# Performance work log

Hardware: AMD Instinct MI355X
Metric: run time of the kernel (lower is better)

Reference implementation:

```python
import jax, jax.numpy as jnp
import numpy as np

FS = 16000.0
Q = 2.0
MAX_MFC = 150.0
LP_CUTOFF = 2.5
ATT_FACTOR = 1.0  # dau1997 preset


def _mfc_array():
    # mfc = 0 (lowpass), 5, 10 Hz linear, then log-spaced with ratio r up to max_mfc
    mfc = [0.0, 5.0, 10.0]
    r = (1.0 + 1.0 / (2.0 * Q)) / (1.0 - 1.0 / (2.0 * Q))  # = 5/3 for Q=2
    f = 10.0 * r
    while f <= MAX_MFC:
        mfc.append(f)
        f *= r
    return np.array(mfc, dtype=np.float64)  # 8 entries for the defaults


def _butter2_lp(fcut, fs):
    # 2nd-order Butterworth lowpass via bilinear transform (matches scipy.signal.butter)
    K = np.tan(np.pi * fcut / fs)
    n = 1.0 / (1.0 + np.sqrt(2.0) * K + K * K)
    b = np.array([K * K, 2.0 * K * K, K * K]) * n
    a = np.array([1.0, 2.0 * (K * K - 1.0) * n, (1.0 - np.sqrt(2.0) * K + K * K) * n])
    return b, a


def setup_inputs() -> dict:
    key = jax.random.key(0)
    x = jax.random.normal(key, (4, 31, 48000), dtype=jnp.float32)  # [B, F, T]
    return {"x": x}


def reference(x):
    B, F, T = x.shape
    N = B * F
    xr = x.reshape(N, T)

    # ---- mfc = 0 filter: 2nd-order Butterworth lowpass @ 2.5 Hz, DF2T scan ----
    b_np, a_np = _butter2_lp(LP_CUTOFF, FS)
    b = jnp.asarray(b_np, jnp.float32)
    a = jnp.asarray(a_np, jnp.float32)

    def lp_step(state, xt):  # state [N,2], xt [N]
        y = b[0] * xt + state[:, 0]
        s0 = b[1] * xt - a[1] * y + state[:, 1]
        s1 = b[2] * xt - a[2] * y
        return jnp.stack([s0, s1], axis=1), y

    _, ylp = jax.lax.scan(lp_step, jnp.zeros((N, 2), jnp.float32), xr.T)
    ylp = 2.0 * ylp.T  # [N, T], factor 2 = 6 dB emphasis

    # ---- bandpass efilt: complex first-order resonators ----
    mfc = _mfc_array()[1:]                      # [M] bandpass center freqs
    bw = np.where(mfc <= 10.0, 5.0, mfc / Q)    # 5 Hz bandwidth for linear part
    e0 = np.exp(-np.pi * bw / FS)               # exp(-(2*pi*bw/fs)/2)
    b0 = jnp.asarray((1.0 - e0).astype(np.complex64))
    cpole = jnp.asarray((e0 * np.exp(1j * 2.0 * np.pi * mfc / FS)).astype(np.complex64))
    M = mfc.shape[0]

    def bp_step(yprev, xt):  # yprev [N,M] complex, xt [N] complex
        y = b0[None, :] * xt[:, None] + cpole[None, :] * yprev
        return y, y

    _, ybp = jax.lax.scan(bp_step, jnp.zeros((N, M), jnp.complex64),
                          xr.T.astype(jnp.complex64))
    ybp = 2.0 * jnp.moveaxis(ybp, 0, -1)        # [N, M, T]

    # phase preserved for mfc <= 10 Hz (real part), envelope (abs) above
    keep_phase = jnp.asarray(mfc <= 10.0)
    out_bp = jnp.where(keep_phase[None, :, None], jnp.real(ybp), ATT_FACTOR * jnp.abs(ybp))

    out = jnp.concatenate([ylp[:, None, :], out_bp], axis=1)  # [N, 1+M, T]
    return out.reshape(B, F, 1 + M, T)
```

## Files before the change

kernel.cpp:

```cpp
#include <hip/hip_runtime.h>
#include <cmath>

#define T_LEN 48000
#define L_CHUNK 128
#define N_CHUNKS 375
#define N_ROWS 124
#define SLOTS 1024
#define ROWS_PER_BLK 64
#define XS_STRIDE 132
#define TR_STRIDE 20
#define GRP 15
#define NGRP 25

struct CoefF {
    float lp_b0, lp_b1, lp_b2, lp_a1, lp_a2;
    float bp_b0[7], bp_cr[7], bp_ci[7];
};
struct CoefD {
    double p00, p01, p10, p11;
    double Pr[7], Pi[7];
};

__device__ __forceinline__ void sel_M(int ch, const CoefD& D,
                                      double& m00, double& m01, double& m10, double& m11) {
    if (ch == 0) {
        m00 = D.p00; m01 = D.p01; m10 = D.p10; m11 = D.p11;
    } else {
        double Pr = 0.0, Pi = 0.0;
#pragma unroll
        for (int c = 1; c < 8; ++c) if (ch == c) { Pr = D.Pr[c - 1]; Pi = D.Pi[c - 1]; }
        m00 = Pr; m01 = -Pi; m10 = Pi; m11 = Pr;
    }
}

template <bool FINAL>
__global__ __launch_bounds__(512) void mfb_chunk(const float* __restrict__ x,
                                                 CoefF C, CoefD D,
                                                 float2* __restrict__ ws_fin,
                                                 const float2* __restrict__ U,
                                                 float* __restrict__ out) {
    extern __shared__ __align__(16) float smem[];
    float* xs = smem;
    const int t     = threadIdx.x;
    const int j     = blockIdx.y;
    const int n0    = (int)blockIdx.x * ROWS_PER_BLK;
    const int tbase = j * L_CHUNK;

#pragma unroll
    for (int i = 0; i < 4; ++i) {
        int g = i * 512 + t;
        int r = g >> 5, c = (g & 31) * 4;
        int n = n0 + r;
        float4 v = make_float4(0.f, 0.f, 0.f, 0.f);
        if (n < N_ROWS)
            v = *reinterpret_cast<const float4*>(x + (size_t)n * T_LEN + tbase + c);
        *reinterpret_cast<float4*>(xs + r * XS_STRIDE + c) = v;
    }
    __syncthreads();

    const int ch   = t >> 6;
    const int nn   = t & 63;
    const int n    = n0 + nn;
    const int slot = ch * 128 + n;
    float* trw = smem + ROWS_PER_BLK * XS_STRIDE + ch * (64 * TR_STRIDE);

    float f_b0, f_b1 = 0.f, f_b2 = 0.f, f_a1 = 0.f, f_a2 = 0.f, f_cr = 0.f, f_ci = 0.f;
    if (ch == 0) {
        f_b0 = C.lp_b0; f_b1 = C.lp_b1; f_b2 = C.lp_b2; f_a1 = C.lp_a1; f_a2 = C.lp_a2;
    } else {
        f_b0 = 0.f;
#pragma unroll
        for (int c = 1; c < 8; ++c)
            if (ch == c) { f_b0 = C.bp_b0[c - 1]; f_cr = C.bp_cr[c - 1]; f_ci = C.bp_ci[c - 1]; }
    }
    const bool kp = (ch <= 2);

    float s0 = 0.f, s1 = 0.f;
    if (FINAL) {
        const int g = j / GRP, i = j - g * GRP;
        double m00, m01, m10, m11;
        sel_M(ch, D, m00, m01, m10, m11);
        float2 ug = U[(size_t)g * SLOTS + slot];
        double u0 = ug.x, u1 = ug.y;
        const float2* Fb = ws_fin + (size_t)(g * GRP) * SLOTS + slot;
        float2 f[GRP - 1];
#pragma unroll
        for (int k = 0; k < GRP - 1; ++k)
            f[k] = (k < i) ? Fb[(size_t)k * SLOTS] : make_float2(0.f, 0.f);
#pragma unroll
        for (int k = 0; k < GRP - 1; ++k)
            if (k < i) {
                double t0 = (double)f[k].x + m00 * u0 + m01 * u1;
                double t1 = (double)f[k].y + m10 * u0 + m11 * u1;
                u0 = t0; u1 = t1;
            }
        s0 = (float)u0; s1 = (float)u1;
    }

    for (int b = 0; b < L_CHUNK / 16; ++b) {
        float4 xv4[4];
#pragma unroll
        for (int q = 0; q < 4; ++q)
            xv4[q] = *reinterpret_cast<const float4*>(xs + nn * XS_STRIDE + b * 16 + q * 4);
        const float* xv = reinterpret_cast<const float*>(xv4);

        float buf[16];
        if (ch == 0) {
#pragma unroll
            for (int k = 0; k < 16; ++k) {
                float xvk = xv[k];
                float y  = fmaf(f_b0, xvk, s0);
                s0 = fmaf(f_b1, xvk, fmaf(-f_a1, y, s1));
                s1 = fmaf(f_b2, xvk, -f_a2 * y);
                if (FINAL) buf[k] = 2.0f * y;
            }
        } else {
#pragma unroll
            for (int k = 0; k < 16; ++k) {
                float xvk = xv[k];
                float nyr = fmaf(f_cr, s0, fmaf(-f_ci, s1, f_b0 * xvk));
                float nyi = fmaf(f_cr, s1, f_ci * s0);
                s0 = nyr; s1 = nyi;
                if (FINAL)
                    buf[k] = kp ? 2.0f * nyr : 2.0f * sqrtf(fmaf(nyr, nyr, nyi * nyi));
            }
        }

        if (FINAL) {
            asm volatile("" ::: "memory");
            *reinterpret_cast<float4*>(trw + nn * TR_STRIDE + 0)  = make_float4(buf[0], buf[1], buf[2], buf[3]);
            *reinterpret_cast<float4*>(trw + nn * TR_STRIDE + 4)  = make_float4(buf[4], buf[5], buf[6], buf[7]);
            *reinterpret_cast<float4*>(trw + nn * TR_STRIDE + 8)  = make_float4(buf[8], buf[9], buf[10], buf[11]);
            *reinterpret_cast<float4*>(trw + nn * TR_STRIDE + 12) = make_float4(buf[12], buf[13], buf[14], buf[15]);
            asm volatile("" ::: "memory");
#pragma unroll
            for (int s = 0; s < 4; ++s) {
                int rr = s * 16 + (nn >> 2);
                int kk = (nn & 3) * 4;
                int nrow = n0 + rr;
                if (nrow < N_ROWS) {
                    float4 v = *reinterpret_cast<const float4*>(trw + rr * TR_STRIDE + kk);
                    *reinterpret_cast<float4*>(out + (size_t)(nrow * 8 + ch) * T_LEN
                                               + tbase + b * 16 + kk) = v;
                }
            }
        }
    }
    if (!FINAL) ws_fin[(size_t)j * SLOTS + slot] = make_float2(s0, s1);
}

__global__ __launch_bounds__(256) void mfb_groupsum(const float2* __restrict__ ws_fin,
                                                    float2* __restrict__ A, CoefD D) {
    int tid = blockIdx.x * 256 + (int)threadIdx.x;
    int s = tid & 1023, g = tid >> 10;
    double m00, m01, m10, m11;
    sel_M(s >> 7, D, m00, m01, m10, m11);

    const float2* base = ws_fin + (size_t)g * GRP * SLOTS + s;
    float2 f[GRP];
#pragma unroll
    for (int i = 0; i < GRP; ++i) f[i] = base[(size_t)i * SLOTS];

    double a0 = 0.0, a1 = 0.0;
#pragma unroll
    for (int i = 0; i < GRP; ++i) {
        double t0 = m00 * a0 + m01 * a1 + (double)f[i].x;
        double t1 = m10 * a0 + m11 * a1 + (double)f[i].y;
        a0 = t0; a1 = t1;
    }
    A[(size_t)g * SLOTS + s] = make_float2((float)a0, (float)a1);
}

__global__ __launch_bounds__(256) void mfb_groupscan(const float2* __restrict__ A,
                                                     float2* __restrict__ U, CoefD D15) {
    int s = blockIdx.x * 256 + (int)threadIdx.x;
    double m00, m01, m10, m11;
    sel_M(s >> 7, D15, m00, m01, m10, m11);

    float2 f[NGRP];
#pragma unroll
    for (int g = 0; g < NGRP; ++g) f[g] = A[(size_t)g * SLOTS + s];

    double u0 = 0.0, u1 = 0.0;
#pragma unroll
    for (int g = 0; g < NGRP; ++g) {
        U[(size_t)g * SLOTS + s] = make_float2((float)u0, (float)u1);
        double t0 = (double)f[g].x + m00 * u0 + m01 * u1;
        double t1 = (double)f[g].y + m10 * u0 + m11 * u1;
        u0 = t0; u1 = t1;
    }
}

extern "C" void kernel_launch(void* const* d_in, const int* in_sizes, int n_in,
                              void* d_out, int out_size, void* d_ws, size_t ws_size,
                              hipStream_t stream) {
    const float* x = (const float*)d_in[0];
    float* out = (float*)d_out;
    char* ws = (char*)d_ws;
    float2* ws_fin  = (float2*)ws;
    float2* Agg     = (float2*)(ws + 3072000);
    float2* Upre    = (float2*)(ws + 3276800);

    const double PI = 3.141592653589793;
    const double FS = 16000.0;
    CoefF C; CoefD D, D15;
    {
        double K   = tan(PI * 2.5 / FS);
        double nrm = 1.0 / (1.0 + sqrt(2.0) * K + K * K);
        double a1  = 2.0 * (K * K - 1.0) * nrm;
        double a2  = (1.0 - sqrt(2.0) * K + K * K) * nrm;
        C.lp_b0 = (float)(K * K * nrm);
        C.lp_b1 = (float)(2.0 * K * K * nrm);
        C.lp_b2 = (float)(K * K * nrm);
        C.lp_a1 = (float)a1;
        C.lp_a2 = (float)a2;
        double p00 = -a1, p01 = 1.0, p10 = -a2, p11 = 0.0;
        for (int i = 0; i < 7; ++i) {
            double q00 = p00 * p00 + p01 * p10, q01 = p00 * p01 + p01 * p11;
            double q10 = p10 * p00 + p11 * p10, q11 = p10 * p01 + p11 * p11;
            p00 = q00; p01 = q01; p10 = q10; p11 = q11;
        }
        D.p00 = p00; D.p01 = p01; D.p10 = p10; D.p11 = p11;
        double r00 = 1, r01 = 0, r10 = 0, r11 = 1, b00 = p00, b01 = p01, b10 = p10, b11 = p11;
        for (int e = 15; e > 0; e >>= 1) {
            if (e & 1) {
                double q00 = r00 * b00 + r01 * b10, q01 = r00 * b01 + r01 * b11;
                double q10 = r10 * b00 + r11 * b10, q11 = r10 * b01 + r11 * b11;
                r00 = q00; r01 = q01; r10 = q10; r11 = q11;
            }
            double q00 = b00 * b00 + b01 * b10, q01 = b00 * b01 + b01 * b11;
            double q10 = b10 * b00 + b11 * b10, q11 = b10 * b01 + b11 * b11;
            b00 = q00; b01 = q01; b10 = q10; b11 = q11;
        }
        D15.p00 = r00; D15.p01 = r01; D15.p10 = r10; D15.p11 = r11;

        double rr = (1.0 + 1.0 / 4.0) / (1.0 - 1.0 / 4.0);
        double mfc[7]; mfc[0] = 5.0; mfc[1] = 10.0;
        double f = 10.0 * rr;
        for (int m = 2; m < 7; ++m) { mfc[m] = f; f *= rr; }
        for (int m = 0; m < 7; ++m) {
            double bw = (mfc[m] <= 10.0) ? 5.0 : mfc[m] * 0.5;
            double e0 = exp(-PI * bw / FS);
            double th = 2.0 * PI * mfc[m] / FS;
            C.bp_b0[m] = (float)(1.0 - e0);
            C.bp_cr[m] = (float)(e0 * cos(th));
            C.bp_ci[m] = (float)(e0 * sin(th));
            double eL  = exp(-PI * bw * (double)L_CHUNK / FS);
            double ang = th * (double)L_CHUNK;
            D.Pr[m] = eL * cos(ang);
            D.Pi[m] = eL * sin(ang);
            double eG  = exp(-PI * bw * (double)(L_CHUNK * GRP) / FS);
            double angG = th * (double)(L_CHUNK * GRP);
            D15.Pr[m] = eG * cos(angG);
            D15.Pi[m] = eG * sin(angG);
        }
    }

    const int smem1 = ROWS_PER_BLK * XS_STRIDE * 4;
    const int smem3 = smem1 + 8 * 64 * TR_STRIDE * 4;
    dim3 grid(2, N_CHUNKS);
    mfb_chunk<false><<<grid, 512, smem1, stream>>>(x, C, D, ws_fin, nullptr, nullptr);
    mfb_groupsum<<<100, 256, 0, stream>>>(ws_fin, Agg, D);
    mfb_groupscan<<<4, 256, 0, stream>>>(Agg, Upre, D15);
    mfb_chunk<true><<<grid, 512, smem3, stream>>>(x, C, D, ws_fin, Upre, out);
}
```

Baseline: 69.96 us.

## Restructure output pass so each wave writes long contiguous runs per stream

The final pass is split into its own kernel. Each 64-lane wave now handles one (row, channel) stream over a window of 64 consecutive chunks, with one lane per chunk. It reads x directly from global with register double-buffering, stages results in LDS, and then writes 32 KB contiguous float4 runs per output row. The old scheme wrote only 64-byte fragments per row per step. The change targets output write coalescing and removes the shared x tile and the template branching. In exchange, x loads become strided per lane, and tail lanes in the last window sit idle.

```diff
diff --git a/kernel.cpp b/kernel.cpp
--- a/kernel.cpp
+++ b/kernel.cpp
@@ -8,9 +8,12 @@
 #define SLOTS 1024
 #define ROWS_PER_BLK 64
 #define XS_STRIDE 132
-#define TR_STRIDE 20
+#define TILE_STRIDE 132
 #define GRP 15
 #define NGRP 25
+#define N_STREAM 992
+#define N_WIN 6
+#define WIN 64
 
 struct CoefF {
     float lp_b0, lp_b1, lp_b2, lp_a1, lp_a2;
@@ -33,12 +36,23 @@
     }
 }
 
-template <bool FINAL>
-__global__ __launch_bounds__(512) void mfb_chunk(const float* __restrict__ x,
-                                                 CoefF C, CoefD D,
-                                                 float2* __restrict__ ws_fin,
-                                                 const float2* __restrict__ U,
-                                                 float* __restrict__ out) {
+__device__ __forceinline__ void sel_coef(int ch, const CoefF& C,
+                                         float& b0, float& b1, float& b2, float& a1,
+                                         float& a2, float& cr, float& ci) {
+    b1 = b2 = a1 = a2 = cr = ci = 0.f;
+    if (ch == 0) {
+        b0 = C.lp_b0; b1 = C.lp_b1; b2 = C.lp_b2; a1 = C.lp_a1; a2 = C.lp_a2;
+    } else {
+        b0 = 0.f;
+#pragma unroll
+        for (int c = 1; c < 8; ++c)
+            if (ch == c) { b0 = C.bp_b0[c - 1]; cr = C.bp_cr[c - 1]; ci = C.bp_ci[c - 1]; }
+    }
+}
+
+__global__ __launch_bounds__(512) void mfb_p1(const float* __restrict__ x,
+                                              CoefF C,
+                                              float2* __restrict__ ws_fin) {
     extern __shared__ __align__(16) float smem[];
     float* xs = smem;
     const int t     = threadIdx.x;
@@ -58,25 +72,101 @@
     }
     __syncthreads();
 
-    const int ch   = t >> 6;
-    const int nn   = t & 63;
-    const int n    = n0 + nn;
+    const int ch = t >> 6, nn = t & 63;
+    const int n  = n0 + nn;
+
+    float f_b0, f_b1, f_b2, f_a1, f_a2, f_cr, f_ci;
+    sel_coef(ch, C, f_b0, f_b1, f_b2, f_a1, f_a2, f_cr, f_ci);
+
+    float s0 = 0.f, s1 = 0.f;
+    for (int b = 0; b < L_CHUNK / 16; ++b) {
+        float4 xv4[4];
+#pragma unroll
+        for (int q = 0; q < 4; ++q)
+            xv4[q] = *reinterpret_cast<const float4*>(xs + nn * XS_STRIDE + b * 16 + q * 4);
+        const float* xv = reinterpret_cast<const float*>(xv4);
+        if (ch == 0) {
+#pragma unroll
+            for (int k = 0; k < 16; ++k) {
+                float xvk = xv[k];
+                float y  = fmaf(f_b0, xvk, s0);
+                s0 = fmaf(f_b1, xvk, fmaf(-f_a1, y, s1));
+                s1 = fmaf(f_b2, xvk, -f_a2 * y);
+            }
+        } else {
+#pragma unroll
+            for (int k = 0; k < 16; ++k) {
+                float xvk = xv[k];
+                float nyr = fmaf(f_cr, s0, fmaf(-f_ci, s1, f_b0 * xvk));
+                float nyi = fmaf(f_cr, s1, f_ci * s0);
+                s0 = nyr; s1 = nyi;
+            }
+        }
+    }
+    ws_fin[(size_t)j * SLOTS + ch * 128 + n] = make_float2(s0, s1);
+}
+
+__global__ __launch_bounds__(256) void mfb_groupsum(const float2* __restrict__ ws_fin,
+                                                    float2* __restrict__ A, CoefD D) {
+    int tid = blockIdx.x * 256 + (int)threadIdx.x;
+    int s = tid & 1023, g = tid >> 10;
+    double m00, m01, m10, m11;
+    sel_M(s >> 7, D, m00, m01, m10, m11);
+    const float2* base = ws_fin + (size_t)g * GRP * SLOTS + s;
+    float2 f[GRP];
+#pragma unroll
+    for (int i = 0; i < GRP; ++i) f[i] = base[(size_t)i * SLOTS];
+    double a0 = 0.0, a1 = 0.0;
+#pragma unroll
+    for (int i = 0; i < GRP; ++i) {
+        double t0 = m00 * a0 + m01 * a1 + (double)f[i].x;
+        double t1 = m10 * a0 + m11 * a1 + (double)f[i].y;
+        a0 = t0; a1 = t1;
+    }
+    A[(size_t)g * SLOTS + s] = make_float2((float)a0, (float)a1);
+}
+
+__global__ __launch_bounds__(256) void mfb_groupscan(const float2* __restrict__ A,
+                                                     float2* __restrict__ U, CoefD D15) {
+    int s = blockIdx.x * 256 + (int)threadIdx.x;
+    double m00, m01, m10, m11;
+    sel_M(s >> 7, D15, m00, m01, m10, m11);
+    float2 f[NGRP];
+#pragma unroll
+    for (int g = 0; g < NGRP; ++g) f[g] = A[(size_t)g * SLOTS + s];
+    double u0 = 0.0, u1 = 0.0;
+#pragma unroll
+    for (int g = 0; g < NGRP; ++g) {
+        U[(size_t)g * SLOTS + s] = make_float2((float)u0, (float)u1);
+        double t0 = (double)f[g].x + m00 * u0 + m01 * u1;
+        double t1 = (double)f[g].y + m10 * u0 + m11 * u1;
+        u0 = t0; u1 = t1;
+    }
+}
+
+__global__ __launch_bounds__(128) void mfb_out(const float* __restrict__ x,
+                                               CoefF C, CoefD D,
+                                               const float2* __restrict__ ws_fin,
+                                               const float2* __restrict__ U,
+                                               float* __restrict__ out) {
+    extern __shared__ __align__(16) float smem[];
+    const int wv = (int)threadIdx.x >> 6, L = (int)threadIdx.x & 63;
+    const int unit = (int)blockIdx.x * 2 + wv;
+    float* tile = smem + wv * (WIN * TILE_STRIDE);
+
+    const int sid = unit / N_WIN;
+    const int w   = unit - sid * N_WIN;
+    const int n   = sid >> 3, ch = sid & 7;
     const int slot = ch * 128 + n;
-    float* trw = smem + ROWS_PER_BLK * XS_STRIDE + ch * (64 * TR_STRIDE);
-
-    float f_b0, f_b1 = 0.f, f_b2 = 0.f, f_a1 = 0.f, f_a2 = 0.f, f_cr = 0.f, f_ci = 0.f;
-    if (ch == 0) {
-        f_b0 = C.lp_b0; f_b1 = C.lp_b1; f_b2 = C.lp_b2; f_a1 = C.lp_a1; f_a2 = C.lp_a2;
-    } else {
-        f_b0 = 0.f;
-#pragma unroll
-        for (int c = 1; c < 8; ++c)
-            if (ch == c) { f_b0 = C.bp_b0[c - 1]; f_cr = C.bp_cr[c - 1]; f_ci = C.bp_ci[c - 1]; }
-    }
+    const int j   = w * WIN + L;
+    const bool act = j < N_CHUNKS;
+
+    float f_b0, f_b1, f_b2, f_a1, f_a2, f_cr, f_ci;
+    sel_coef(ch, C, f_b0, f_b1, f_b2, f_a1, f_a2, f_cr, f_ci);
     const bool kp = (ch <= 2);
 
     float s0 = 0.f, s1 = 0.f;
-    if (FINAL) {
+    if (act) {
         const int g = j / GRP, i = j - g * GRP;
         double m00, m01, m10, m11;
         sel_M(ch, D, m00, m01, m10, m11);
@@ -97,13 +187,21 @@
         s0 = (float)u0; s1 = (float)u1;
     }
 
-    for (int b = 0; b < L_CHUNK / 16; ++b) {
-        float4 xv4[4];
+    const float* xrow = x + (size_t)n * T_LEN + (size_t)j * L_CHUNK;
+    float4 cur[4] = {};
+    if (act) {
 #pragma unroll
         for (int q = 0; q < 4; ++q)
-            xv4[q] = *reinterpret_cast<const float4*>(xs + nn * XS_STRIDE + b * 16 + q * 4);
-        const float* xv = reinterpret_cast<const float*>(xv4);
-
+            cur[q] = *reinterpret_cast<const float4*>(xrow + q * 4);
+    }
+    for (int b = 0; b < 8; ++b) {
+        float4 nxt[4] = {};
+        if (act && b < 7) {
+#pragma unroll
+            for (int q = 0; q < 4; ++q)
+                nxt[q] = *reinterpret_cast<const float4*>(xrow + (b + 1) * 16 + q * 4);
+        }
+        const float* xv = reinterpret_cast<const float*>(cur);
         float buf[16];
         if (ch == 0) {
 #pragma unroll
@@ -112,7 +210,7 @@
                 float y  = fmaf(f_b0, xvk, s0);
                 s0 = fmaf(f_b1, xvk, fmaf(-f_a1, y, s1));
                 s1 = fmaf(f_b2, xvk, -f_a2 * y);
-                if (FINAL) buf[k] = 2.0f * y;
+                buf[k] = 2.0f * y;
             }
         } else {
 #pragma unroll
@@ -121,73 +219,30 @@
                 float nyr = fmaf(f_cr, s0, fmaf(-f_ci, s1, f_b0 * xvk));
                 float nyi = fmaf(f_cr, s1, f_ci * s0);
                 s0 = nyr; s1 = nyi;
-                if (FINAL)
-                    buf[k] = kp ? 2.0f * nyr : 2.0f * sqrtf(fmaf(nyr, nyr, nyi * nyi));
-            }
-        }
-
-        if (FINAL) {
-            asm volatile("" ::: "memory");
-            *reinterpret_cast<float4*>(trw + nn * TR_STRIDE + 0)  = make_float4(buf[0], buf[1], buf[2], buf[3]);
-            *reinterpret_cast<float4*>(trw + nn * TR_STRIDE + 4)  = make_float4(buf[4], buf[5], buf[6], buf[7]);
-            *reinterpret_cast<float4*>(trw + nn * TR_STRIDE + 8)  = make_float4(buf[8], buf[9], buf[10], buf[11]);
-            *reinterpret_cast<float4*>(trw + nn * TR_STRIDE + 12) = make_float4(buf[12], buf[13], buf[14], buf[15]);
-            asm volatile("" ::: "memory");
-#pragma unroll
-            for (int s = 0; s < 4; ++s) {
-                int rr = s * 16 + (nn >> 2);
-                int kk = (nn & 3) * 4;
-                int nrow = n0 + rr;
-                if (nrow < N_ROWS) {
-                    float4 v = *reinterpret_cast<const float4*>(trw + rr * TR_STRIDE + kk);
-                    *reinterpret_cast<float4*>(out + (size_t)(nrow * 8 + ch) * T_LEN
-                                               + tbase + b * 16 + kk) = v;
-                }
-            }
-        }
-    }
-    if (!FINAL) ws_fin[(size_t)j * SLOTS + slot] = make_float2(s0, s1);
-}
-
-__global__ __launch_bounds__(256) void mfb_groupsum(const float2* __restrict__ ws_fin,
-                                                    float2* __restrict__ A, CoefD D) {
-    int tid = blockIdx.x * 256 + (int)threadIdx.x;
-    int s = tid & 1023, g = tid >> 10;
-    double m00, m01, m10, m11;
-    sel_M(s >> 7, D, m00, m01, m10, m11);
-
-    const float2* base = ws_fin + (size_t)g * GRP * SLOTS + s;
-    float2 f[GRP];
-#pragma unroll
-    for (int i = 0; i < GRP; ++i) f[i] = base[(size_t)i * SLOTS];
-
-    double a0 = 0.0, a1 = 0.0;
-#pragma unroll
-    for (int i = 0; i < GRP; ++i) {
-        double t0 = m00 * a0 + m01 * a1 + (double)f[i].x;
-        double t1 = m10 * a0 + m11 * a1 + (double)f[i].y;
-        a0 = t0; a1 = t1;
-    }
-    A[(size_t)g * SLOTS + s] = make_float2((float)a0, (float)a1);
-}
-
-__global__ __launch_bounds__(256) void mfb_groupscan(const float2* __restrict__ A,
-                                                     float2* __restrict__ U, CoefD D15) {
-    int s = blockIdx.x * 256 + (int)threadIdx.x;
-    double m00, m01, m10, m11;
-    sel_M(s >> 7, D15, m00, m01, m10, m11);
-
-    float2 f[NGRP];
-#pragma unroll
-    for (int g = 0; g < NGRP; ++g) f[g] = A[(size_t)g * SLOTS + s];
-
-    double u0 = 0.0, u1 = 0.0;
-#pragma unroll
-    for (int g = 0; g < NGRP; ++g) {
-        U[(size_t)g * SLOTS + s] = make_float2((float)u0, (float)u1);
-        double t0 = (double)f[g].x + m00 * u0 + m01 * u1;
-        double t1 = (double)f[g].y + m10 * u0 + m11 * u1;
-        u0 = t0; u1 = t1;
+                buf[k] = kp ? 2.0f * nyr : 2.0f * sqrtf(fmaf(nyr, nyr, nyi * nyi));
+            }
+        }
+        float* tr = tile + L * TILE_STRIDE + b * 16;
+        *reinterpret_cast<float4*>(tr + 0)  = make_float4(buf[0], buf[1], buf[2], buf[3]);
+        *reinterpret_cast<float4*>(tr + 4)  = make_float4(buf[4], buf[5], buf[6], buf[7]);
+        *reinterpret_cast<float4*>(tr + 8)  = make_float4(buf[8], buf[9], buf[10], buf[11]);
+        *reinterpret_cast<float4*>(tr + 12) = make_float4(buf[12], buf[13], buf[14], buf[15]);
+#pragma unroll
+        for (int q = 0; q < 4; ++q) cur[q] = nxt[q];
+    }
+
+    asm volatile("" ::: "memory");
+
+    const int tw0 = w * (WIN * L_CHUNK);
+    float* orow = out + (size_t)sid * T_LEN;
+    for (int d = 0; d < 32; ++d) {
+        int tloc = d * 256 + L * 4;
+        int t = tw0 + tloc;
+        if (t < T_LEN) {
+            float4 v = *reinterpret_cast<const float4*>(
+                tile + ((tloc >> 7) * TILE_STRIDE) + (tloc & 127));
+            *reinterpret_cast<float4*>(orow + t) = v;
+        }
     }
 }
 
@@ -257,10 +312,10 @@
     }
 
     const int smem1 = ROWS_PER_BLK * XS_STRIDE * 4;
-    const int smem3 = smem1 + 8 * 64 * TR_STRIDE * 4;
-    dim3 grid(2, N_CHUNKS);
-    mfb_chunk<false><<<grid, 512, smem1, stream>>>(x, C, D, ws_fin, nullptr, nullptr);
+    const int smem3 = 2 * WIN * TILE_STRIDE * 4;
+    dim3 grid1(2, N_CHUNKS);
+    mfb_p1<<<grid1, 512, smem1, stream>>>(x, C, ws_fin);
     mfb_groupsum<<<100, 256, 0, stream>>>(ws_fin, Agg, D);
     mfb_groupscan<<<4, 256, 0, stream>>>(Agg, Upre, D15);
-    mfb_chunk<true><<<grid, 512, smem3, stream>>>(x, C, D, ws_fin, Upre, out);
-}
+    mfb_out<<<(N_STREAM * N_WIN) / 2, 128, smem3, stream>>>(x, C, D, ws_fin, Upre, out);
+}
```

Result: slower. 135.7 us (+94.0%).

## Merge group-sum and group-scan kernels with grid barrier; hoist carry loads; nontemporal stores

Applied to the files above, without the earlier changes.

Replaces the two small carry-propagation kernels with a single 32-block kernel that computes the group aggregates, synchronizes all blocks through an atomic grid barrier, then runs the scan across groups, removing one launch. It also issues the carry/prefix loads in the final chunk pass before the input tile load so their latency overlaps, and writes output with nontemporal stores. A memset is added each call to reset the barrier counters. The barrier relies on all 32 blocks being co-resident.

```diff
diff --git a/kernel.cpp b/kernel.cpp
--- a/kernel.cpp
+++ b/kernel.cpp
@@ -11,6 +11,9 @@
 #define TR_STRIDE 20
 #define GRP 15
 #define NGRP 25
+#define TREE_BLOCKS 32
+
+typedef float f32x4 __attribute__((ext_vector_type(4)));
 
 struct CoefF {
     float lp_b0, lp_b1, lp_b2, lp_a1, lp_a2;
@@ -31,6 +34,23 @@
         for (int c = 1; c < 8; ++c) if (ch == c) { Pr = D.Pr[c - 1]; Pi = D.Pi[c - 1]; }
         m00 = Pr; m01 = -Pi; m10 = Pi; m11 = Pr;
     }
+}
+
+__device__ __forceinline__ void grid_barrier(unsigned* bar, unsigned nb) {
+    __syncthreads();
+    if (threadIdx.x == 0) {
+        unsigned g = __hip_atomic_load(&bar[1], __ATOMIC_RELAXED, __HIP_MEMORY_SCOPE_AGENT);
+        unsigned a = __hip_atomic_fetch_add(&bar[0], 1u, __ATOMIC_RELEASE, __HIP_MEMORY_SCOPE_AGENT);
+        if (a == nb - 1u) {
+            __hip_atomic_store(&bar[0], 0u, __ATOMIC_RELAXED, __HIP_MEMORY_SCOPE_AGENT);
+            __hip_atomic_fetch_add(&bar[1], 1u, __ATOMIC_RELEASE, __HIP_MEMORY_SCOPE_AGENT);
+        } else {
+            while (__hip_atomic_load(&bar[1], __ATOMIC_RELAXED, __HIP_MEMORY_SCOPE_AGENT) == g)
+                __builtin_amdgcn_s_sleep(16);
+        }
+        __builtin_amdgcn_fence(__ATOMIC_ACQUIRE, "agent");
+    }
+    __syncthreads();
 }
 
 template <bool FINAL>
@@ -46,22 +66,35 @@
     const int n0    = (int)blockIdx.x * ROWS_PER_BLK;
     const int tbase = j * L_CHUNK;
 
-#pragma unroll
-    for (int i = 0; i < 4; ++i) {
-        int g = i * 512 + t;
-        int r = g >> 5, c = (g & 31) * 4;
-        int n = n0 + r;
-        float4 v = make_float4(0.f, 0.f, 0.f, 0.f);
-        if (n < N_ROWS)
-            v = *reinterpret_cast<const float4*>(x + (size_t)n * T_LEN + tbase + c);
-        *reinterpret_cast<float4*>(xs + r * XS_STRIDE + c) = v;
-    }
-    __syncthreads();
-
     const int ch   = t >> 6;
     const int nn   = t & 63;
     const int n    = n0 + nn;
     const int slot = ch * 128 + n;
+
+    float2 ug = make_float2(0.f, 0.f);
+    float2 f[GRP - 1];
+    int ii = 0;
+    if (FINAL) {
+        const int gg = j / GRP; ii = j - gg * GRP;
+        ug = U[(size_t)gg * SLOTS + slot];
+        const float2* Fb = ws_fin + (size_t)(gg * GRP) * SLOTS + slot;
+#pragma unroll
+        for (int k = 0; k < GRP - 1; ++k)
+            f[k] = (k < ii) ? Fb[(size_t)k * SLOTS] : make_float2(0.f, 0.f);
+    }
+
+#pragma unroll
+    for (int i = 0; i < 4; ++i) {
+        int g = i * 512 + t;
+        int r = g >> 5, c = (g & 31) * 4;
+        int nr = n0 + r;
+        float4 v = make_float4(0.f, 0.f, 0.f, 0.f);
+        if (nr < N_ROWS)
+            v = *reinterpret_cast<const float4*>(x + (size_t)nr * T_LEN + tbase + c);
+        *reinterpret_cast<float4*>(xs + r * XS_STRIDE + c) = v;
+    }
+    __syncthreads();
+
     float* trw = smem + ROWS_PER_BLK * XS_STRIDE + ch * (64 * TR_STRIDE);
 
     float f_b0, f_b1 = 0.f, f_b2 = 0.f, f_a1 = 0.f, f_a2 = 0.f, f_cr = 0.f, f_ci = 0.f;
@@ -77,19 +110,12 @@
 
     float s0 = 0.f, s1 = 0.f;
     if (FINAL) {
-        const int g = j / GRP, i = j - g * GRP;
         double m00, m01, m10, m11;
         sel_M(ch, D, m00, m01, m10, m11);
-        float2 ug = U[(size_t)g * SLOTS + slot];
         double u0 = ug.x, u1 = ug.y;
-        const float2* Fb = ws_fin + (size_t)(g * GRP) * SLOTS + slot;
-        float2 f[GRP - 1];
 #pragma unroll
         for (int k = 0; k < GRP - 1; ++k)
-            f[k] = (k < i) ? Fb[(size_t)k * SLOTS] : make_float2(0.f, 0.f);
-#pragma unroll
-        for (int k = 0; k < GRP - 1; ++k)
-            if (k < i) {
+            if (k < ii) {
                 double t0 = (double)f[k].x + m00 * u0 + m01 * u1;
                 double t1 = (double)f[k].y + m10 * u0 + m11 * u1;
                 u0 = t0; u1 = t1;
@@ -139,9 +165,10 @@
                 int kk = (nn & 3) * 4;
                 int nrow = n0 + rr;
                 if (nrow < N_ROWS) {
-                    float4 v = *reinterpret_cast<const float4*>(trw + rr * TR_STRIDE + kk);
-                    *reinterpret_cast<float4*>(out + (size_t)(nrow * 8 + ch) * T_LEN
-                                               + tbase + b * 16 + kk) = v;
+                    f32x4 v = *reinterpret_cast<const f32x4*>(trw + rr * TR_STRIDE + kk);
+                    __builtin_nontemporal_store(v,
+                        reinterpret_cast<f32x4*>(out + (size_t)(nrow * 8 + ch) * T_LEN
+                                                 + tbase + b * 16 + kk));
                 }
             }
         }
@@ -149,45 +176,51 @@
     if (!FINAL) ws_fin[(size_t)j * SLOTS + slot] = make_float2(s0, s1);
 }
 
-__global__ __launch_bounds__(256) void mfb_groupsum(const float2* __restrict__ ws_fin,
-                                                    float2* __restrict__ A, CoefD D) {
-    int tid = blockIdx.x * 256 + (int)threadIdx.x;
-    int s = tid & 1023, g = tid >> 10;
-    double m00, m01, m10, m11;
-    sel_M(s >> 7, D, m00, m01, m10, m11);
-
-    const float2* base = ws_fin + (size_t)g * GRP * SLOTS + s;
-    float2 f[GRP];
-#pragma unroll
-    for (int i = 0; i < GRP; ++i) f[i] = base[(size_t)i * SLOTS];
-
-    double a0 = 0.0, a1 = 0.0;
-#pragma unroll
-    for (int i = 0; i < GRP; ++i) {
-        double t0 = m00 * a0 + m01 * a1 + (double)f[i].x;
-        double t1 = m10 * a0 + m11 * a1 + (double)f[i].y;
-        a0 = t0; a1 = t1;
-    }
-    A[(size_t)g * SLOTS + s] = make_float2((float)a0, (float)a1);
-}
-
-__global__ __launch_bounds__(256) void mfb_groupscan(const float2* __restrict__ A,
-                                                     float2* __restrict__ U, CoefD D15) {
-    int s = blockIdx.x * 256 + (int)threadIdx.x;
-    double m00, m01, m10, m11;
-    sel_M(s >> 7, D15, m00, m01, m10, m11);
-
-    float2 f[NGRP];
-#pragma unroll
-    for (int g = 0; g < NGRP; ++g) f[g] = A[(size_t)g * SLOTS + s];
-
-    double u0 = 0.0, u1 = 0.0;
-#pragma unroll
-    for (int g = 0; g < NGRP; ++g) {
-        U[(size_t)g * SLOTS + s] = make_float2((float)u0, (float)u1);
-        double t0 = (double)f[g].x + m00 * u0 + m01 * u1;
-        double t1 = (double)f[g].y + m10 * u0 + m11 * u1;
-        u0 = t0; u1 = t1;
+__global__ __launch_bounds__(256) void mfb_tree(const float2* __restrict__ ws_fin,
+                                                float2* __restrict__ Agg,
+                                                float2* __restrict__ U,
+                                                CoefD D, CoefD D15,
+                                                unsigned* __restrict__ bar) {
+    const int tid = (int)blockIdx.x * 256 + (int)threadIdx.x;
+
+    for (int r = 0; r < 4; ++r) {
+        int job = r * 8192 + tid;
+        if (job < SLOTS * NGRP) {
+            int s = job & 1023, g = job >> 10;
+            double m00, m01, m10, m11;
+            sel_M(s >> 7, D, m00, m01, m10, m11);
+            const float2* base = ws_fin + (size_t)g * GRP * SLOTS + s;
+            float2 f[GRP];
+#pragma unroll
+            for (int i = 0; i < GRP; ++i) f[i] = base[(size_t)i * SLOTS];
+            double a0 = 0.0, a1 = 0.0;
+#pragma unroll
+            for (int i = 0; i < GRP; ++i) {
+                double t0 = m00 * a0 + m01 * a1 + (double)f[i].x;
+                double t1 = m10 * a0 + m11 * a1 + (double)f[i].y;
+                a0 = t0; a1 = t1;
+            }
+            Agg[(size_t)g * SLOTS + s] = make_float2((float)a0, (float)a1);
+        }
+    }
+
+    grid_barrier(bar, TREE_BLOCKS);
+
+    if (tid < SLOTS) {
+        int s = tid;
+        double m00, m01, m10, m11;
+        sel_M(s >> 7, D15, m00, m01, m10, m11);
+        float2 f[NGRP];
+#pragma unroll
+        for (int g = 0; g < NGRP; ++g) f[g] = Agg[(size_t)g * SLOTS + s];
+        double u0 = 0.0, u1 = 0.0;
+#pragma unroll
+        for (int g = 0; g < NGRP; ++g) {
+            U[(size_t)g * SLOTS + s] = make_float2((float)u0, (float)u1);
+            double t0 = (double)f[g].x + m00 * u0 + m01 * u1;
+            double t1 = (double)f[g].y + m10 * u0 + m11 * u1;
+            u0 = t0; u1 = t1;
+        }
     }
 }
 
@@ -200,6 +233,7 @@
     float2* ws_fin  = (float2*)ws;
     float2* Agg     = (float2*)(ws + 3072000);
     float2* Upre    = (float2*)(ws + 3276800);
+    unsigned* bar   = (unsigned*)(ws + 3481600);
 
     const double PI = 3.141592653589793;
     const double FS = 16000.0;
@@ -259,8 +293,8 @@
     const int smem1 = ROWS_PER_BLK * XS_STRIDE * 4;
     const int smem3 = smem1 + 8 * 64 * TR_STRIDE * 4;
     dim3 grid(2, N_CHUNKS);
+    (void)hipMemsetAsync(bar, 0, 8, stream);
     mfb_chunk<false><<<grid, 512, smem1, stream>>>(x, C, D, ws_fin, nullptr, nullptr);
-    mfb_groupsum<<<100, 256, 0, stream>>>(ws_fin, Agg, D);
-    mfb_groupscan<<<4, 256, 0, stream>>>(Agg, Upre, D15);
+    mfb_tree<<<TREE_BLOCKS, 256, 0, stream>>>(ws_fin, Agg, Upre, D, D15, bar);
     mfb_chunk<true><<<grid, 512, smem3, stream>>>(x, C, D, ws_fin, Upre, out);
 }
```

Result: slower. 98.24 us (+40.4%).

## Split final scan pass into 32-sample subchunks with per-row window blocks

Applied to the files above, without the earlier changes.

The first pass now also saves filter states at every 32-sample boundary within each 128-sample chunk. The output pass is rebuilt so that each block handles one row and a 2048-sample window, with one channel per wave. Each thread now runs only 32 serial steps instead of 128, and output goes through a swizzled shared-memory tile for coalesced stores. This shortens the serial dependency chain and raises parallelism in the output kernel. In exchange it adds extra workspace traffic for the intermediate states and more double-precision prefix fixup per thread.

```diff
diff --git a/kernel.cpp b/kernel.cpp
--- a/kernel.cpp
+++ b/kernel.cpp
@@ -8,9 +8,11 @@
 #define SLOTS 1024
 #define ROWS_PER_BLK 64
 #define XS_STRIDE 132
-#define TR_STRIDE 20
 #define GRP 15
 #define NGRP 25
+#define SUB 32
+#define WPW 2048
+#define N_WIN 24
 
 struct CoefF {
     float lp_b0, lp_b1, lp_b2, lp_a1, lp_a2;
@@ -33,12 +35,9 @@
     }
 }
 
-template <bool FINAL>
-__global__ __launch_bounds__(512) void mfb_chunk(const float* __restrict__ x,
-                                                 CoefF C, CoefD D,
-                                                 float2* __restrict__ ws_fin,
-                                                 const float2* __restrict__ U,
-                                                 float* __restrict__ out) {
+__global__ __launch_bounds__(512) void mfb_p1(const float* __restrict__ x, CoefF C,
+                                              float2* __restrict__ ws_fin,
+                                              float2* __restrict__ wsS) {
     extern __shared__ __align__(16) float smem[];
     float* xs = smem;
     const int t     = threadIdx.x;
@@ -58,11 +57,9 @@
     }
     __syncthreads();
 
-    const int ch   = t >> 6;
-    const int nn   = t & 63;
-    const int n    = n0 + nn;
+    const int ch = t >> 6, nn = t & 63;
+    const int n  = n0 + nn;
     const int slot = ch * 128 + n;
-    float* trw = smem + ROWS_PER_BLK * XS_STRIDE + ch * (64 * TR_STRIDE);
 
     float f_b0, f_b1 = 0.f, f_b2 = 0.f, f_a1 = 0.f, f_a2 = 0.f, f_cr = 0.f, f_ci = 0.f;
     if (ch == 0) {
@@ -73,11 +70,121 @@
         for (int c = 1; c < 8; ++c)
             if (ch == c) { f_b0 = C.bp_b0[c - 1]; f_cr = C.bp_cr[c - 1]; f_ci = C.bp_ci[c - 1]; }
     }
+
+    float s0 = 0.f, s1 = 0.f;
+    for (int b = 0; b < 8; ++b) {
+        float4 xv4[4];
+#pragma unroll
+        for (int q = 0; q < 4; ++q)
+            xv4[q] = *reinterpret_cast<const float4*>(xs + nn * XS_STRIDE + b * 16 + q * 4);
+        const float* xv = reinterpret_cast<const float*>(xv4);
+        if (ch == 0) {
+#pragma unroll
+            for (int k = 0; k < 16; ++k) {
+                float xvk = xv[k];
+                float y  = fmaf(f_b0, xvk, s0);
+                s0 = fmaf(f_b1, xvk, fmaf(-f_a1, y, s1));
+                s1 = fmaf(f_b2, xvk, -f_a2 * y);
+            }
+        } else {
+#pragma unroll
+            for (int k = 0; k < 16; ++k) {
+                float xvk = xv[k];
+                float nyr = fmaf(f_cr, s0, fmaf(-f_ci, s1, f_b0 * xvk));
+                float nyi = fmaf(f_cr, s1, f_ci * s0);
+                s0 = nyr; s1 = nyi;
+            }
+        }
+        if (b == 1 || b == 3 || b == 5)
+            wsS[(size_t)(j * 3 + (b >> 1)) * SLOTS + slot] = make_float2(s0, s1);
+    }
+    ws_fin[(size_t)j * SLOTS + slot] = make_float2(s0, s1);
+}
+
+__global__ __launch_bounds__(256) void mfb_groupsum(const float2* __restrict__ ws_fin,
+                                                    float2* __restrict__ A, CoefD D) {
+    int tid = blockIdx.x * 256 + (int)threadIdx.x;
+    int s = tid & 1023, g = tid >> 10;
+    double m00, m01, m10, m11;
+    sel_M(s >> 7, D, m00, m01, m10, m11);
+    const float2* base = ws_fin + (size_t)g * GRP * SLOTS + s;
+    float2 f[GRP];
+#pragma unroll
+    for (int i = 0; i < GRP; ++i) f[i] = base[(size_t)i * SLOTS];
+    double a0 = 0.0, a1 = 0.0;
+#pragma unroll
+    for (int i = 0; i < GRP; ++i) {
+        double t0 = m00 * a0 + m01 * a1 + (double)f[i].x;
+        double t1 = m10 * a0 + m11 * a1 + (double)f[i].y;
+        a0 = t0; a1 = t1;
+    }
+    A[(size_t)g * SLOTS + s] = make_float2((float)a0, (float)a1);
+}
+
+__global__ __launch_bounds__(256) void mfb_groupscan(const float2* __restrict__ A,
+                                                     float2* __restrict__ U, CoefD D15) {
+    int s = blockIdx.x * 256 + (int)threadIdx.x;
+    double m00, m01, m10, m11;
+    sel_M(s >> 7, D15, m00, m01, m10, m11);
+    float2 f[NGRP];
+#pragma unroll
+    for (int g = 0; g < NGRP; ++g) f[g] = A[(size_t)g * SLOTS + s];
+    double u0 = 0.0, u1 = 0.0;
+#pragma unroll
+    for (int g = 0; g < NGRP; ++g) {
+        U[(size_t)g * SLOTS + s] = make_float2((float)u0, (float)u1);
+        double t0 = (double)f[g].x + m00 * u0 + m01 * u1;
+        double t1 = (double)f[g].y + m10 * u0 + m11 * u1;
+        u0 = t0; u1 = t1;
+    }
+}
+
+__global__ __launch_bounds__(512) void mfb_out(const float* __restrict__ x,
+                                               CoefF C, CoefD D, CoefD E1, CoefD D32_unused_pad,
+                                               const float2* __restrict__ ws_fin,
+                                               const float2* __restrict__ wsS,
+                                               const float2* __restrict__ U,
+                                               float* __restrict__ out) {
+    extern __shared__ __align__(16) float smem[];
+    float* xsub = smem;
+    const int t  = threadIdx.x;
+    const int wv = t >> 6, L = t & 63;
+    const int bid = (int)blockIdx.x;
+    const int n = bid / N_WIN, w = bid - n * N_WIN;
+    const int ch = wv;
+    const int slot = ch * 128 + n;
+    float* tile = smem + 64 * 32 + wv * (64 * 32);
+
+    {
+        int p = t * 4;
+        int off = w * WPW + p;
+        float4 v = make_float4(0.f, 0.f, 0.f, 0.f);
+        if (off < T_LEN)
+            v = *reinterpret_cast<const float4*>(x + (size_t)n * T_LEN + off);
+        int row = p >> 5;
+        int col = (p & 31) ^ ((row & 7) << 2);
+        *reinterpret_cast<float4*>(xsub + row * 32 + col) = v;
+    }
+    __syncthreads();
+
+    const bool act = (w * WPW + L * SUB) < T_LEN;
+
+    float f_b0, f_b1 = 0.f, f_b2 = 0.f, f_a1 = 0.f, f_a2 = 0.f, f_cr = 0.f, f_ci = 0.f;
+    if (ch == 0) {
+        f_b0 = C.lp_b0; f_b1 = C.lp_b1; f_b2 = C.lp_b2; f_a1 = C.lp_a1; f_a2 = C.lp_a2;
+    } else {
+        f_b0 = 0.f;
+#pragma unroll
+        for (int c = 1; c < 8; ++c)
+            if (ch == c) { f_b0 = C.bp_b0[c - 1]; f_cr = C.bp_cr[c - 1]; f_ci = C.bp_ci[c - 1]; }
+    }
     const bool kp = (ch <= 2);
 
     float s0 = 0.f, s1 = 0.f;
-    if (FINAL) {
-        const int g = j / GRP, i = j - g * GRP;
+    if (act) {
+        const int j128 = w * 16 + (L >> 2);
+        const int r    = L & 3;
+        const int g = j128 / GRP, i = j128 - g * GRP;
         double m00, m01, m10, m11;
         sel_M(ch, D, m00, m01, m10, m11);
         float2 ug = U[(size_t)g * SLOTS + slot];
@@ -94,100 +201,73 @@
                 double t1 = (double)f[k].y + m10 * u0 + m11 * u1;
                 u0 = t0; u1 = t1;
             }
+        double e00, e01, e10, e11;
+        sel_M(ch, E1, e00, e01, e10, e11);
+#pragma unroll
+        for (int k = 0; k < 3; ++k)
+            if (k < r) {
+                double t0 = e00 * u0 + e01 * u1;
+                double t1 = e10 * u0 + e11 * u1;
+                u0 = t0; u1 = t1;
+            }
+        if (r) {
+            float2 sr = wsS[(size_t)(j128 * 3 + (r - 1)) * SLOTS + slot];
+            u0 += (double)sr.x; u1 += (double)sr.y;
+        }
         s0 = (float)u0; s1 = (float)u1;
     }
 
-    for (int b = 0; b < L_CHUNK / 16; ++b) {
-        float4 xv4[4];
-#pragma unroll
-        for (int q = 0; q < 4; ++q)
-            xv4[q] = *reinterpret_cast<const float4*>(xs + nn * XS_STRIDE + b * 16 + q * 4);
-        const float* xv = reinterpret_cast<const float*>(xv4);
-
-        float buf[16];
+    const int swz = (L & 7) << 2;
+    if (act) {
         if (ch == 0) {
 #pragma unroll
-            for (int k = 0; k < 16; ++k) {
-                float xvk = xv[k];
-                float y  = fmaf(f_b0, xvk, s0);
-                s0 = fmaf(f_b1, xvk, fmaf(-f_a1, y, s1));
-                s1 = fmaf(f_b2, xvk, -f_a2 * y);
-                if (FINAL) buf[k] = 2.0f * y;
+            for (int q = 0; q < 8; ++q) {
+                float4 xv = *reinterpret_cast<const float4*>(xsub + L * 32 + ((q * 4) ^ swz));
+                float o[4];
+                const float* xp = reinterpret_cast<const float*>(&xv);
+#pragma unroll
+                for (int k = 0; k < 4; ++k) {
+                    float xvk = xp[k];
+                    float y  = fmaf(f_b0, xvk, s0);
+                    s0 = fmaf(f_b1, xvk, fmaf(-f_a1, y, s1));
+                    s1 = fmaf(f_b2, xvk, -f_a2 * y);
+                    o[k] = 2.0f * y;
+                }
+                *reinterpret_cast<float4*>(tile + L * 32 + ((q * 4) ^ swz)) =
+                    make_float4(o[0], o[1], o[2], o[3]);
             }
         } else {
 #pragma unroll
-            for (int k = 0; k < 16; ++k) {
-                float xvk = xv[k];
-                float nyr = fmaf(f_cr, s0, fmaf(-f_ci, s1, f_b0 * xvk));
-                float nyi = fmaf(f_cr, s1, f_ci * s0);
-                s0 = nyr; s1 = nyi;
-                if (FINAL)
-                    buf[k] = kp ? 2.0f * nyr : 2.0f * sqrtf(fmaf(nyr, nyr, nyi * nyi));
-            }
-        }
-
-        if (FINAL) {
-            asm volatile("" ::: "memory");
-            *reinterpret_cast<float4*>(trw + nn * TR_STRIDE + 0)  = make_float4(buf[0], buf[1], buf[2], buf[3]);
-            *reinterpret_cast<float4*>(trw + nn * TR_STRIDE + 4)  = make_float4(buf[4], buf[5], buf[6], buf[7]);
-            *reinterpret_cast<float4*>(trw + nn * TR_STRIDE + 8)  = make_float4(buf[8], buf[9], buf[10], buf[11]);
-            *reinterpret_cast<float4*>(trw + nn * TR_STRIDE + 12) = make_float4(buf[12], buf[13], buf[14], buf[15]);
-            asm volatile("" ::: "memory");
-#pragma unroll
-            for (int s = 0; s < 4; ++s) {
-                int rr = s * 16 + (nn >> 2);
-                int kk = (nn & 3) * 4;
-                int nrow = n0 + rr;
-                if (nrow < N_ROWS) {
-                    float4 v = *reinterpret_cast<const float4*>(trw + rr * TR_STRIDE + kk);
-                    *reinterpret_cast<float4*>(out + (size_t)(nrow * 8 + ch) * T_LEN
-                                               + tbase + b * 16 + kk) = v;
+            for (int q = 0; q < 8; ++q) {
+                float4 xv = *reinterpret_cast<const float4*>(xsub + L * 32 + ((q * 4) ^ swz));
+                float o[4];
+                const float* xp = reinterpret_cast<const float*>(&xv);
+#pragma unroll
+                for (int k = 0; k < 4; ++k) {
+                    float xvk = xp[k];
+                    float nyr = fmaf(f_cr, s0, fmaf(-f_ci, s1, f_b0 * xvk));
+                    float nyi = fmaf(f_cr, s1, f_ci * s0);
+                    s0 = nyr; s1 = nyi;
+                    o[k] = kp ? 2.0f * nyr : 2.0f * sqrtf(fmaf(nyr, nyr, nyi * nyi));
                 }
-            }
-        }
-    }
-    if (!FINAL) ws_fin[(size_t)j * SLOTS + slot] = make_float2(s0, s1);
-}
-
-__global__ __launch_bounds__(256) void mfb_groupsum(const float2* __restrict__ ws_fin,
-                                                    float2* __restrict__ A, CoefD D) {
-    int tid = blockIdx.x * 256 + (int)threadIdx.x;
-    int s = tid & 1023, g = tid >> 10;
-    double m00, m01, m10, m11;
-    sel_M(s >> 7, D, m00, m01, m10, m11);
-
-    const float2* base = ws_fin + (size_t)g * GRP * SLOTS + s;
-    float2 f[GRP];
-#pragma unroll
-    for (int i = 0; i < GRP; ++i) f[i] = base[(size_t)i * SLOTS];
-
-    double a0 = 0.0, a1 = 0.0;
-#pragma unroll
-    for (int i = 0; i < GRP; ++i) {
-        double t0 = m00 * a0 + m01 * a1 + (double)f[i].x;
-        double t1 = m10 * a0 + m11 * a1 + (double)f[i].y;
-        a0 = t0; a1 = t1;
-    }
-    A[(size_t)g * SLOTS + s] = make_float2((float)a0, (float)a1);
-}
-
-__global__ __launch_bounds__(256) void mfb_groupscan(const float2* __restrict__ A,
-                                                     float2* __restrict__ U, CoefD D15) {
-    int s = blockIdx.x * 256 + (int)threadIdx.x;
-    double m00, m01, m10, m11;
-    sel_M(s >> 7, D15, m00, m01, m10, m11);
-
-    float2 f[NGRP];
-#pragma unroll
-    for (int g = 0; g < NGRP; ++g) f[g] = A[(size_t)g * SLOTS + s];
-
-    double u0 = 0.0, u1 = 0.0;
-#pragma unroll
-    for (int g = 0; g < NGRP; ++g) {
-        U[(size_t)g * SLOTS + s] = make_float2((float)u0, (float)u1);
-        double t0 = (double)f[g].x + m00 * u0 + m01 * u1;
-        double t1 = (double)f[g].y + m10 * u0 + m11 * u1;
-        u0 = t0; u1 = t1;
+                *reinterpret_cast<float4*>(tile + L * 32 + ((q * 4) ^ swz)) =
+                    make_float4(o[0], o[1], o[2], o[3]);
+            }
+        }
+    }
+
+    asm volatile("" ::: "memory");
+
+    float* orow = out + (size_t)(n * 8 + ch) * T_LEN + w * WPW;
+#pragma unroll
+    for (int d = 0; d < 8; ++d) {
+        int idx = d * 256 + L * 4;
+        if (w * WPW + idx < T_LEN) {
+            int row = idx >> 5;
+            int col = (idx & 31) ^ ((row & 7) << 2);
+            float4 v = *reinterpret_cast<const float4*>(tile + row * 32 + col);
+            *reinterpret_cast<float4*>(orow + idx) = v;
+        }
     }
 }
 
@@ -197,13 +277,14 @@
     const float* x = (const float*)d_in[0];
     float* out = (float*)d_out;
     char* ws = (char*)d_ws;
-    float2* ws_fin  = (float2*)ws;
-    float2* Agg     = (float2*)(ws + 3072000);
-    float2* Upre    = (float2*)(ws + 3276800);
+    float2* ws_fin = (float2*)ws;
+    float2* wsS    = (float2*)(ws + 3072000);
+    float2* Agg    = (float2*)(ws + 12288000);
+    float2* Upre   = (float2*)(ws + 12492800);
 
     const double PI = 3.141592653589793;
     const double FS = 16000.0;
-    CoefF C; CoefD D, D15;
+    CoefF C; CoefD D, D15, E1;
     {
         double K   = tan(PI * 2.5 / FS);
         double nrm = 1.0 / (1.0 + sqrt(2.0) * K + K * K);
@@ -215,7 +296,13 @@
         C.lp_a1 = (float)a1;
         C.lp_a2 = (float)a2;
         double p00 = -a1, p01 = 1.0, p10 = -a2, p11 = 0.0;
-        for (int i = 0; i < 7; ++i) {
+        for (int i = 0; i < 5; ++i) {
+            double q00 = p00 * p00 + p01 * p10, q01 = p00 * p01 + p01 * p11;
+            double q10 = p10 * p00 + p11 * p10, q11 = p10 * p01 + p11 * p11;
+            p00 = q00; p01 = q01; p10 = q10; p11 = q11;
+        }
+        E1.p00 = p00; E1.p01 = p01; E1.p10 = p10; E1.p11 = p11;
+        for (int i = 0; i < 2; ++i) {
             double q00 = p00 * p00 + p01 * p10, q01 = p00 * p01 + p01 * p11;
             double q10 = p10 * p00 + p11 * p10, q11 = p10 * p01 + p11 * p11;
             p00 = q00; p01 = q01; p10 = q10; p11 = q11;
@@ -253,14 +340,19 @@
             double angG = th * (double)(L_CHUNK * GRP);
             D15.Pr[m] = eG * cos(angG);
             D15.Pi[m] = eG * sin(angG);
+            double e32 = exp(-PI * bw * (double)SUB / FS);
+            double a32 = th * (double)SUB;
+            E1.Pr[m] = e32 * cos(a32);
+            E1.Pi[m] = e32 * sin(a32);
         }
     }
 
     const int smem1 = ROWS_PER_BLK * XS_STRIDE * 4;
-    const int smem3 = smem1 + 8 * 64 * TR_STRIDE * 4;
-    dim3 grid(2, N_CHUNKS);
-    mfb_chunk<false><<<grid, 512, smem1, stream>>>(x, C, D, ws_fin, nullptr, nullptr);
+    const int smem3 = 9 * 64 * 32 * 4;
+    dim3 grid1(2, N_CHUNKS);
+    mfb_p1<<<grid1, 512, smem1, stream>>>(x, C, ws_fin, wsS);
     mfb_groupsum<<<100, 256, 0, stream>>>(ws_fin, Agg, D);
     mfb_groupscan<<<4, 256, 0, stream>>>(Agg, Upre, D15);
-    mfb_chunk<true><<<grid, 512, smem3, stream>>>(x, C, D, ws_fin, Upre, out);
-}
+    mfb_out<<<N_ROWS * N_WIN, 512, smem3, stream>>>(x, C, D, E1, D15,
+                                                    ws_fin, wsS, Upre, out);
+}
```

Result: slower. 87.03 us (+24.4%).
